# Kernel tuning notes

Measured on AMD Instinct MI355X. Metric: run time of the kernel, lower is better.

Reference implementation:

```python
import jax, jax.numpy as jnp
import numpy as np
from jax import lax

DN = ('NCHW', 'OIHW', 'NCHW')

def _dwsep(x, dw, pw_w, pw_b, stride):
    # depthwise: groups = in_channels, kernel (C,1,3,3)
    y = lax.conv_general_dilated(x, dw, (stride, stride), [(1, 1), (1, 1)],
                                 dimension_numbers=DN, feature_group_count=x.shape[1])
    # pointwise 1x1
    y = lax.conv_general_dilated(y, pw_w, (1, 1), 'VALID', dimension_numbers=DN)
    return y + pw_b[None, :, None, None]

def setup_inputs() -> dict:
    key = jax.random.key(0)
    ks = jax.random.split(key, 16)
    s = 0.1
    inp = {
        'flow_raw': jax.random.normal(ks[0], (32, 2, 480, 640), jnp.float32),
        'dw1': jax.random.normal(ks[1], (5, 1, 3, 3), jnp.float32) * s,
        'pw1_w': jax.random.normal(ks[2], (32, 5, 1, 1), jnp.float32) * s,
        'pw1_b': jnp.zeros((32,), jnp.float32),
        'dw2': jax.random.normal(ks[3], (32, 1, 3, 3), jnp.float32) * s,
        'pw2_w': jax.random.normal(ks[4], (64, 32, 1, 1), jnp.float32) * s,
        'pw2_b': jnp.zeros((64,), jnp.float32),
        'dw3': jax.random.normal(ks[5], (64, 1, 3, 3), jnp.float32) * s,
        'pw3_w': jax.random.normal(ks[6], (64, 64, 1, 1), jnp.float32) * s,
        'pw3_b': jnp.zeros((64,), jnp.float32),
        'attn_w': jax.random.normal(ks[7], (1, 64, 1, 1), jnp.float32) * s,
        'attn_b': jnp.zeros((1,), jnp.float32),
        'mlp1_w': jax.random.normal(ks[8], (32, 64), jnp.float32) * s,
        'mlp1_b': jnp.zeros((32,), jnp.float32),
        'mlp2_w': jax.random.normal(ks[9], (3, 32), jnp.float32) * s,
        'mlp2_b': jnp.zeros((3,), jnp.float32),
        'w_ih': jax.random.normal(ks[10], (96, 3), jnp.float32) * s,
        'w_hh': jax.random.normal(ks[11], (96, 32), jnp.float32) * s,
        'b_ih': jnp.zeros((96,), jnp.float32),
        'b_hh': jnp.zeros((96,), jnp.float32),
        'fc_w': jnp.zeros((3, 32), jnp.float32),  # gru_fc init to zero in torch code
        'fc_b': jnp.zeros((3,), jnp.float32),
    }
    return inp

def reference(flow_raw, dw1, pw1_w, pw1_b, dw2, pw2_w, pw2_b, dw3, pw3_w, pw3_b,
              attn_w, attn_b, mlp1_w, mlp1_b, mlp2_w, mlp2_b,
              w_ih, w_hh, b_ih, b_hh, fc_w, fc_b):
    B, _, H, W = flow_raw.shape
    # coordinate channels (x, y, r^2)
    y = jnp.linspace(-1.0, 1.0, H)
    x = jnp.linspace(-1.0, 1.0, W)
    yy, xx = jnp.meshgrid(y, x, indexing='ij')
    coords = jnp.stack([xx, yy, xx**2 + yy**2], axis=0)            # (3,H,W)
    coords_b = jnp.broadcast_to(coords[None], (B, 3, H, W))
    inp = jnp.concatenate([flow_raw, coords_b], axis=1)            # (B,5,H,W)

    f = jax.nn.elu(_dwsep(inp, dw1, pw1_w, pw1_b, 2))              # (B,32,H/2,W/2)
    f = jax.nn.elu(_dwsep(f, dw2, pw2_w, pw2_b, 2))                # (B,64,H/4,W/4)
    f = jax.nn.elu(_dwsep(f, dw3, pw3_w, pw3_b, 2))                # (B,64,H/8,W/8)

    # attention pooling
    logits = jnp.einsum('bchw,oc->bohw', f, attn_w[:, :, 0, 0]) + attn_b[None, :, None, None]
    Bs, _, Hs, Ws = logits.shape
    w = jax.nn.softmax(logits.reshape(Bs, Hs * Ws), axis=-1)       # (B, HW)
    pooled = jnp.einsum('bcn,bn->bc', f.reshape(Bs, 64, Hs * Ws), w)  # (B,64)

    # omega MLP
    h1 = jax.nn.elu(pooled @ mlp1_w.T + mlp1_b)
    omega_inst = h1 @ mlp2_w.T + mlp2_b                            # (B,3)

    # single-step GRU, h0 = 0 (PyTorch gate order: r, z, n)
    h0 = jnp.zeros((B, 32), flow_raw.dtype)
    gi = omega_inst @ w_ih.T + b_ih                                # (B,96)
    gh = h0 @ w_hh.T + b_hh
    i_r, i_z, i_n = jnp.split(gi, 3, axis=-1)
    h_r, h_z, h_n = jnp.split(gh, 3, axis=-1)
    r = jax.nn.sigmoid(i_r + h_r)
    z = jax.nn.sigmoid(i_z + h_z)
    n = jnp.tanh(i_n + r * h_n)
    h = (1.0 - z) * n + z * h0                                     # (B,32)

    delta_omega = h @ fc_w.T + fc_b
    return omega_inst + delta_omega
```

## Files before the change

kernel.cpp:

```cpp
#include <hip/hip_runtime.h>
#include <hip/hip_bf16.h>

#define H0 480
#define W0 640
#define H1 240
#define W1 320
#define H2 120
#define W2 160
#define H3 60
#define W3 80

#define W_PW1T  0
#define W_PW2T  160
#define W_PW3T  2208
#define WBUF_BYTES 65536

#define F2_PB (64 * H2 * W2)
#define F3_PB (64 * H3 * W3)

__global__ __launch_bounds__(256) void k_cvt(
    const float* __restrict__ pw1, const float* __restrict__ pw2,
    const float* __restrict__ pw3, float* __restrict__ wb)
{
    int t = threadIdx.x;
    for (int i = t; i < 160;  i += 256) { int o = i / 5,  c = i % 5;  wb[W_PW1T + c*32 + o] = pw1[i]; }
    for (int i = t; i < 2048; i += 256) { int o = i >> 5, c = i & 31; wb[W_PW2T + c*64 + o] = pw2[i]; }
    for (int i = t; i < 4096; i += 256) { int o = i >> 6, c = i & 63; wb[W_PW3T + c*64 + o] = pw3[i]; }
}

__global__ __launch_bounds__(256, 3) void k_fuse12(
    const float* __restrict__ flow, const float* __restrict__ dw1,
    const float* __restrict__ b1, const float* __restrict__ dw2,
    const float* __restrict__ b2, const float* __restrict__ wb,
    float* __restrict__ out)
{
    int idx = blockIdx.x * 256 + threadIdx.x;
    int ow = idx % W2; int tmp = idx / W2; int oh = tmp % H2; int b = tmp / H2;

    int fh0 = 2*oh - 1, fw0 = 2*ow - 1;
    const float sy = 2.f / (H0 - 1), sx = 2.f / (W0 - 1);

    float d[9][5];
    float vm[9];

    #pragma unroll
    for (int r = 0; r < 3; r++) {
        #pragma unroll
        for (int s = 0; s < 3; s++) {
            int p = r*3 + s;
            int fh = fh0 + r, fw = fw0 + s;
            vm[p] = (fh >= 0 && fw >= 0) ? 1.f : 0.f;
            int fhc = fh < 0 ? 0 : fh, fwc = fw < 0 ? 0 : fw;
            int ih0 = 2*fhc - 1, iw0 = 2*fwc - 1;
            float mh[3] = { ih0 >= 0 ? 1.f : 0.f, 1.f, 1.f };
            float mw[3] = { iw0 >= 0 ? 1.f : 0.f, 1.f, 1.f };
            int ihx[3] = { ih0 < 0 ? 0 : ih0, ih0 + 1, ih0 + 2 };
            int iwx[3] = { iw0 < 0 ? 0 : iw0, iw0 + 1, iw0 + 2 };

            #pragma unroll
            for (int c = 0; c < 2; c++) {
                const float* base = flow + ((size_t)(b*2 + c)) * (H0*W0);
                float a = 0.f;
                #pragma unroll
                for (int ky = 0; ky < 3; ky++) {
                    const float* rp = base + (size_t)ihx[ky] * W0;
                    #pragma unroll
                    for (int kx = 0; kx < 3; kx++)
                        a = fmaf(dw1[c*9 + ky*3 + kx], (mh[ky]*mw[kx]) * rp[iwx[kx]], a);
                }
                d[p][c] = a;
            }
            float ax = 0.f, ay = 0.f, ar = 0.f;
            #pragma unroll
            for (int ky = 0; ky < 3; ky++) {
                float yv = fmaf((float)(ih0 + ky), sy, -1.f);
                #pragma unroll
                for (int kx = 0; kx < 3; kx++) {
                    float xv = fmaf((float)(iw0 + kx), sx, -1.f);
                    float m = mh[ky] * mw[kx];
                    ax = fmaf(dw1[18 + ky*3 + kx], m * xv, ax);
                    ay = fmaf(dw1[27 + ky*3 + kx], m * yv, ay);
                    ar = fmaf(dw1[36 + ky*3 + kx], m * (xv*xv + yv*yv), ar);
                }
            }
            d[p][2] = ax; d[p][3] = ay; d[p][4] = ar;
        }
    }

    float acc[64];
    #pragma unroll
    for (int o = 0; o < 64; o++) acc[o] = b2[o];

    for (int c = 0; c < 32; c++) {
        const float* w1 = wb + W_PW1T + c;
        float w10 = w1[0], w11 = w1[32], w12 = w1[64], w13 = w1[96], w14 = w1[128];
        float bc = b1[c];
        const float* w9 = dw2 + c*9;
        float dv = 0.f;
        #pragma unroll
        for (int p = 0; p < 9; p++) {
            float v = bc;
            v = fmaf(w10, d[p][0], v);
            v = fmaf(w11, d[p][1], v);
            v = fmaf(w12, d[p][2], v);
            v = fmaf(w13, d[p][3], v);
            v = fmaf(w14, d[p][4], v);
            float f1v = v > 0.f ? v : (__expf(v) - 1.f);
            dv = fmaf(w9[p], f1v * vm[p], dv);
        }
        const float* wr = wb + W_PW2T + c*64;
        #pragma unroll
        for (int o = 0; o < 64; o++) acc[o] = fmaf(wr[o], dv, acc[o]);
    }

    size_t obase = ((size_t)b * 64) * (H2*W2) + (size_t)oh*W2 + ow;
    #pragma unroll
    for (int o = 0; o < 64; o++) {
        float v = acc[o];
        out[obase + (size_t)o*(H2*W2)] = v > 0.f ? v : (__expf(v) - 1.f);
    }
}

__global__ __launch_bounds__(256, 4) void k_stage3(
    const float* __restrict__ in, const float* __restrict__ dw3,
    const float* __restrict__ b3, const float* __restrict__ wb,
    float* __restrict__ out)
{
    int idx = blockIdx.x * 256 + threadIdx.x;
    int ow = idx % W3; int tmp = idx / W3; int oh = tmp % H3; int b = tmp / H3;
    int ih0 = 2*oh - 1, iw0 = 2*ow - 1;
    float mh[3] = { ih0 >= 0 ? 1.f : 0.f, 1.f, 1.f };
    float mw[3] = { iw0 >= 0 ? 1.f : 0.f, 1.f, 1.f };
    int ihx[3] = { ih0 < 0 ? 0 : ih0, ih0 + 1, ih0 + 2 };
    int iwx[3] = { iw0 < 0 ? 0 : iw0, iw0 + 1, iw0 + 2 };
    float m9[9];
    int off[9];
    #pragma unroll
    for (int ky = 0; ky < 3; ky++)
        #pragma unroll
        for (int kx = 0; kx < 3; kx++) {
            m9[ky*3 + kx] = mh[ky] * mw[kx];
            off[ky*3 + kx] = ihx[ky]*W2 + iwx[kx];
        }

    float acc[64];
    #pragma unroll
    for (int o = 0; o < 64; o++) acc[o] = b3[o];

    const float* inb = in + (size_t)b * F2_PB;
    for (int c = 0; c < 64; c++) {
        const float* g = inb + (size_t)c * (H2*W2);
        const float* w9 = dw3 + c*9;
        float dv = 0.f;
        #pragma unroll
        for (int p = 0; p < 9; p++)
            dv = fmaf(w9[p], m9[p] * g[off[p]], dv);
        const float* wr = wb + W_PW3T + c*64;
        #pragma unroll
        for (int o = 0; o < 64; o++) acc[o] = fmaf(wr[o], dv, acc[o]);
    }

    size_t obase = ((size_t)b * 64) * (H3*W3) + (size_t)oh*W3 + ow;
    #pragma unroll
    for (int o = 0; o < 64; o++) {
        float v = acc[o];
        out[obase + (size_t)o*(H3*W3)] = v > 0.f ? v : (__expf(v) - 1.f);
    }
}

__global__ __launch_bounds__(1024) void k_head(
    const float* __restrict__ f3,
    const float* __restrict__ attn_w, const float* __restrict__ attn_b,
    const float* __restrict__ mlp1_w, const float* __restrict__ mlp1_b,
    const float* __restrict__ mlp2_w, const float* __restrict__ mlp2_b,
    const float* __restrict__ w_ih, const float* __restrict__ b_ih,
    const float* __restrict__ b_hh,
    const float* __restrict__ fc_w, const float* __restrict__ fc_b,
    float* __restrict__ out)
{
    const int N  = H3 * W3;
    const int N4 = N / 4;
    __shared__ float s_w[H3 * W3];
    __shared__ float s_attn[64];
    __shared__ float s_redm[16];
    __shared__ float s_reds[16];
    __shared__ float s_inv[1];
    __shared__ float s_pooled[64];
    __shared__ float s_h1[32];
    __shared__ float s_om[3];
    __shared__ float s_h[32];

    int t = threadIdx.x, b = blockIdx.x;
    int lane = t & 63, wid = t >> 6;
    if (t < 64) s_attn[t] = attn_w[t];
    __syncthreads();

    const float4* fb4 = (const float4*)(f3 + (size_t)b * F3_PB);
    float ab = attn_b[0];

    float lmax = -1e30f;
    for (int n4 = t; n4 < N4; n4 += 1024) {
        float4 l = make_float4(ab, ab, ab, ab);
        #pragma unroll 8
        for (int c = 0; c < 64; c++) {
            float4 v = fb4[c * N4 + n4];
            float a = s_attn[c];
            l.x = fmaf(a, v.x, l.x); l.y = fmaf(a, v.y, l.y);
            l.z = fmaf(a, v.z, l.z); l.w = fmaf(a, v.w, l.w);
        }
        ((float4*)s_w)[n4] = l;
        lmax = fmaxf(lmax, fmaxf(fmaxf(l.x, l.y), fmaxf(l.z, l.w)));
    }
    #pragma unroll
    for (int off = 32; off; off >>= 1) lmax = fmaxf(lmax, __shfl_down(lmax, off, 64));
    if (lane == 0) s_redm[wid] = lmax;
    __syncthreads();
    {
        float m = s_redm[0];
        #pragma unroll
        for (int i = 1; i < 16; i++) m = fmaxf(m, s_redm[i]);
        lmax = m;
    }

    float lsum = 0.f;
    for (int n = t; n < N; n += 1024) { float e = __expf(s_w[n] - lmax); s_w[n] = e; lsum += e; }
    #pragma unroll
    for (int off = 32; off; off >>= 1) lsum += __shfl_down(lsum, off, 64);
    if (lane == 0) s_reds[wid] = lsum;
    __syncthreads();
    if (t == 0) {
        float s = 0.f;
        #pragma unroll
        for (int i = 0; i < 16; i++) s += s_reds[i];
        s_inv[0] = 1.f / s;
    }
    __syncthreads();
    float invS = s_inv[0];

    const float4* sw4 = (const float4*)s_w;
    for (int c = wid; c < 64; c += 16) {
        float s = 0.f;
        for (int i = lane; i < N4; i += 64) {
            float4 v = fb4[c * N4 + i];
            float4 w = sw4[i];
            s = fmaf(v.x, w.x, s); s = fmaf(v.y, w.y, s);
            s = fmaf(v.z, w.z, s); s = fmaf(v.w, w.w, s);
        }
        #pragma unroll
        for (int off = 32; off; off >>= 1) s += __shfl_down(s, off, 64);
        if (lane == 0) s_pooled[c] = s * invS;
    }
    __syncthreads();

    if (t < 32) {
        float a = mlp1_b[t];
        #pragma unroll 8
        for (int c = 0; c < 64; c++) a = fmaf(mlp1_w[t*64 + c], s_pooled[c], a);
        s_h1[t] = a > 0.f ? a : (__expf(a) - 1.f);
    }
    __syncthreads();
    if (t < 3) {
        float a = mlp2_b[t];
        for (int j = 0; j < 32; j++) a = fmaf(mlp2_w[t*32 + j], s_h1[j], a);
        s_om[t] = a;
    }
    __syncthreads();
    if (t < 32) {
        float gr = b_ih[t], gz = b_ih[32 + t], gn = b_ih[64 + t];
        #pragma unroll
        for (int k = 0; k < 3; k++) {
            float ok = s_om[k];
            gr = fmaf(w_ih[t*3 + k],        ok, gr);
            gz = fmaf(w_ih[(32 + t)*3 + k], ok, gz);
            gn = fmaf(w_ih[(64 + t)*3 + k], ok, gn);
        }
        float hr = b_hh[t], hz = b_hh[32 + t], hn = b_hh[64 + t];
        float r = 1.f / (1.f + __expf(-(gr + hr)));
        float z = 1.f / (1.f + __expf(-(gz + hz)));
        float nn = tanhf(gn + r * hn);
        s_h[t] = (1.f - z) * nn;
    }
    __syncthreads();
    if (t < 3) {
        float dl = fc_b[t];
        for (int j = 0; j < 32; j++) dl = fmaf(fc_w[t*32 + j], s_h[j], dl);
        out[b*3 + t] = s_om[t] + dl;
    }
}

extern "C" void kernel_launch(void* const* d_in, const int* in_sizes, int n_in,
                              void* d_out, int out_size, void* d_ws, size_t ws_size,
                              hipStream_t stream)
{
    const float* flow = (const float*)d_in[0];
    float* wb = (float*)d_ws;

    float* f2 = (float*)((char*)d_ws + WBUF_BYTES);
    float* f3 = f2 + (size_t)32 * F2_PB;

    k_cvt<<<1, 256, 0, stream>>>(
        (const float*)d_in[2], (const float*)d_in[5], (const float*)d_in[8], wb);

    k_fuse12<<<(32*H2*W2)/256, 256, 0, stream>>>(
        flow, (const float*)d_in[1], (const float*)d_in[3],
        (const float*)d_in[4], (const float*)d_in[6], wb, f2);

    k_stage3<<<(32*H3*W3)/256, 256, 0, stream>>>(
        f2, (const float*)d_in[7], (const float*)d_in[9], wb, f3);

    k_head<<<32, 1024, 0, stream>>>(f3,
        (const float*)d_in[10], (const float*)d_in[11],
        (const float*)d_in[12], (const float*)d_in[13],
        (const float*)d_in[14], (const float*)d_in[15],
        (const float*)d_in[16], (const float*)d_in[18],
        (const float*)d_in[19], (const float*)d_in[20],
        (const float*)d_in[21], (float*)d_out);
}
```

Measured before the change: 346.8 us.

## Split interior and border pixels; use packed FMA and factored coordinate convolution

Both conv kernels now remap thread indices so interior output pixels take a branch-free path without padding masks or clamped indices, and border pixels keep the original masked code. In stage 1 the interior path loads a shared 7x7 input window once per channel instead of re-gathering 9 overlapping 3x3 patches, and computes the x/y/r² coordinate-channel convolutions through separable row and column sums. The 64-wide pointwise accumulation uses 2-wide float vectors with elementwise FMA, intended to map to packed FP32 FMA. The cost is a larger code body and divergence inside warps that straddle the interior/border boundary.

Result: slower. 368.1 us (+6.1%).

```diff
diff --git a/kernel.cpp b/kernel.cpp
--- a/kernel.cpp
+++ b/kernel.cpp
@@ -17,6 +17,8 @@
 
 #define F2_PB (64 * H2 * W2)
 #define F3_PB (64 * H3 * W3)
+
+typedef float v2f __attribute__((ext_vector_type(2)));
 
 __global__ __launch_bounds__(256) void k_cvt(
     const float* __restrict__ pw1, const float* __restrict__ pw2,
@@ -35,89 +37,215 @@
     float* __restrict__ out)
 {
     int idx = blockIdx.x * 256 + threadIdx.x;
-    int ow = idx % W2; int tmp = idx / W2; int oh = tmp % H2; int b = tmp / H2;
-
-    int fh0 = 2*oh - 1, fw0 = 2*ow - 1;
+    int t = idx % (H2*W2); int b = idx / (H2*W2);
     const float sy = 2.f / (H0 - 1), sx = 2.f / (W0 - 1);
-
-    float d[9][5];
-    float vm[9];
-
-    #pragma unroll
-    for (int r = 0; r < 3; r++) {
-        #pragma unroll
-        for (int s = 0; s < 3; s++) {
-            int p = r*3 + s;
-            int fh = fh0 + r, fw = fw0 + s;
-            vm[p] = (fh >= 0 && fw >= 0) ? 1.f : 0.f;
-            int fhc = fh < 0 ? 0 : fh, fwc = fw < 0 ? 0 : fw;
-            int ih0 = 2*fhc - 1, iw0 = 2*fwc - 1;
-            float mh[3] = { ih0 >= 0 ? 1.f : 0.f, 1.f, 1.f };
-            float mw[3] = { iw0 >= 0 ? 1.f : 0.f, 1.f, 1.f };
-            int ihx[3] = { ih0 < 0 ? 0 : ih0, ih0 + 1, ih0 + 2 };
-            int iwx[3] = { iw0 < 0 ? 0 : iw0, iw0 + 1, iw0 + 2 };
-
+    const int NI = (H2-1) * (W2-1);
+
+    if (t < NI) {
+        int oh = 1 + t / (W2-1), ow = 1 + t % (W2-1);
+        float d[9][5];
+
+        {
+            const float* a0 = flow + ((size_t)(b*2)) * (H0*W0)
+                              + (size_t)(4*oh - 3) * W0 + (4*ow - 3);
             #pragma unroll
             for (int c = 0; c < 2; c++) {
-                const float* base = flow + ((size_t)(b*2 + c)) * (H0*W0);
-                float a = 0.f;
+                const float* ap = a0 + (size_t)c * (H0*W0);
+                float w[7][7];
+                #pragma unroll
+                for (int r7 = 0; r7 < 7; r7++)
+                    #pragma unroll
+                    for (int k = 0; k < 7; k++)
+                        w[r7][k] = ap[r7*W0 + k];
+                #pragma unroll
+                for (int r = 0; r < 3; r++)
+                    #pragma unroll
+                    for (int s = 0; s < 3; s++) {
+                        float a = 0.f;
+                        #pragma unroll
+                        for (int ky = 0; ky < 3; ky++)
+                            #pragma unroll
+                            for (int kx = 0; kx < 3; kx++)
+                                a = fmaf(dw1[c*9 + ky*3 + kx], w[2*r+ky][2*s+kx], a);
+                        d[r*3+s][c] = a;
+                    }
+            }
+        }
+
+        {
+            float cs2[3], rs3[3], cs4[3], rs4[3];
+            #pragma unroll
+            for (int k = 0; k < 3; k++) {
+                cs2[k] = dw1[18+k]   + dw1[21+k]   + dw1[24+k];
+                rs3[k] = dw1[27+3*k] + dw1[28+3*k] + dw1[29+3*k];
+                cs4[k] = dw1[36+k]   + dw1[39+k]   + dw1[42+k];
+                rs4[k] = dw1[36+3*k] + dw1[37+3*k] + dw1[38+3*k];
+            }
+            float u[7], vv7[7], u2[7], v2a[7];
+            float ub = fmaf((float)(4*ow - 3), sx, -1.f);
+            float vb = fmaf((float)(4*oh - 3), sy, -1.f);
+            #pragma unroll
+            for (int m = 0; m < 7; m++) {
+                u[m]   = fmaf((float)m, sx, ub);
+                vv7[m] = fmaf((float)m, sy, vb);
+                u2[m]  = u[m]*u[m];
+                v2a[m] = vv7[m]*vv7[m];
+            }
+            float axs[3], arx[3], ays[3], ary[3];
+            #pragma unroll
+            for (int s = 0; s < 3; s++) {
+                float ax = 0.f, gx = 0.f;
+                #pragma unroll
+                for (int kx = 0; kx < 3; kx++) {
+                    ax = fmaf(cs2[kx], u[2*s+kx],  ax);
+                    gx = fmaf(cs4[kx], u2[2*s+kx], gx);
+                }
+                axs[s] = ax; arx[s] = gx;
+            }
+            #pragma unroll
+            for (int r = 0; r < 3; r++) {
+                float ay = 0.f, gy = 0.f;
                 #pragma unroll
                 for (int ky = 0; ky < 3; ky++) {
-                    const float* rp = base + (size_t)ihx[ky] * W0;
+                    ay = fmaf(rs3[ky], vv7[2*r+ky], ay);
+                    gy = fmaf(rs4[ky], v2a[2*r+ky], gy);
+                }
+                ays[r] = ay; ary[r] = gy;
+            }
+            #pragma unroll
+            for (int r = 0; r < 3; r++)
+                #pragma unroll
+                for (int s = 0; s < 3; s++) {
+                    d[r*3+s][2] = axs[s];
+                    d[r*3+s][3] = ays[r];
+                    d[r*3+s][4] = arx[s] + ary[r];
+                }
+        }
+
+        v2f acc2[32];
+        #pragma unroll
+        for (int o = 0; o < 32; o++) acc2[o] = *(const v2f*)(b2 + 2*o);
+
+        for (int c = 0; c < 32; c++) {
+            const float* w1 = wb + W_PW1T + c;
+            float w10 = w1[0], w11 = w1[32], w12 = w1[64], w13 = w1[96], w14 = w1[128];
+            float bc = b1[c];
+            const float* w9 = dw2 + c*9;
+            float dv = 0.f;
+            #pragma unroll
+            for (int p = 0; p < 9; p++) {
+                float vv = bc;
+                vv = fmaf(w10, d[p][0], vv);
+                vv = fmaf(w11, d[p][1], vv);
+                vv = fmaf(w12, d[p][2], vv);
+                vv = fmaf(w13, d[p][3], vv);
+                vv = fmaf(w14, d[p][4], vv);
+                float f1v = vv > 0.f ? vv : (__expf(vv) - 1.f);
+                dv = fmaf(w9[p], f1v, dv);
+            }
+            const v2f* wr2 = (const v2f*)(wb + W_PW2T + c*64);
+            v2f dvv = { dv, dv };
+            #pragma unroll
+            for (int o = 0; o < 32; o++)
+                acc2[o] = __builtin_elementwise_fma(wr2[o], dvv, acc2[o]);
+        }
+
+        size_t obase = ((size_t)b * 64) * (H2*W2) + (size_t)oh*W2 + ow;
+        #pragma unroll
+        for (int o = 0; o < 32; o++) {
+            float va = acc2[o].x, vb2 = acc2[o].y;
+            out[obase + (size_t)(2*o)  *(H2*W2)] = va  > 0.f ? va  : (__expf(va)  - 1.f);
+            out[obase + (size_t)(2*o+1)*(H2*W2)] = vb2 > 0.f ? vb2 : (__expf(vb2) - 1.f);
+        }
+        return;
+    }
+
+    {
+        int s2 = t - NI;
+        int oh, ow;
+        if (s2 < W2) { oh = 0; ow = s2; } else { oh = s2 - (W2-1); ow = 0; }
+
+        int fh0 = 2*oh - 1, fw0 = 2*ow - 1;
+
+        float d[9][5];
+        float vm[9];
+
+        #pragma unroll
+        for (int r = 0; r < 3; r++) {
+            #pragma unroll
+            for (int s = 0; s < 3; s++) {
+                int p = r*3 + s;
+                int fh = fh0 + r, fw = fw0 + s;
+                vm[p] = (fh >= 0 && fw >= 0) ? 1.f : 0.f;
+                int fhc = fh < 0 ? 0 : fh, fwc = fw < 0 ? 0 : fw;
+                int ih0 = 2*fhc - 1, iw0 = 2*fwc - 1;
+                float mh[3] = { ih0 >= 0 ? 1.f : 0.f, 1.f, 1.f };
+                float mw[3] = { iw0 >= 0 ? 1.f : 0.f, 1.f, 1.f };
+                int ihx[3] = { ih0 < 0 ? 0 : ih0, ih0 + 1, ih0 + 2 };
+                int iwx[3] = { iw0 < 0 ? 0 : iw0, iw0 + 1, iw0 + 2 };
+
+                #pragma unroll
+                for (int c = 0; c < 2; c++) {
+                    const float* base = flow + ((size_t)(b*2 + c)) * (H0*W0);
+                    float a = 0.f;
                     #pragma unroll
-                    for (int kx = 0; kx < 3; kx++)
-                        a = fmaf(dw1[c*9 + ky*3 + kx], (mh[ky]*mw[kx]) * rp[iwx[kx]], a);
+                    for (int ky = 0; ky < 3; ky++) {
+                        const float* rp = base + (size_t)ihx[ky] * W0;
+                        #pragma unroll
+                        for (int kx = 0; kx < 3; kx++)
+                            a = fmaf(dw1[c*9 + ky*3 + kx], (mh[ky]*mw[kx]) * rp[iwx[kx]], a);
+                    }
+                    d[p][c] = a;
                 }
-                d[p][c] = a;
-            }
-            float ax = 0.f, ay = 0.f, ar = 0.f;
-            #pragma unroll
-            for (int ky = 0; ky < 3; ky++) {
-                float yv = fmaf((float)(ih0 + ky), sy, -1.f);
-                #pragma unroll
-                for (int kx = 0; kx < 3; kx++) {
-                    float xv = fmaf((float)(iw0 + kx), sx, -1.f);
-                    float m = mh[ky] * mw[kx];
-                    ax = fmaf(dw1[18 + ky*3 + kx], m * xv, ax);
-                    ay = fmaf(dw1[27 + ky*3 + kx], m * yv, ay);
-                    ar = fmaf(dw1[36 + ky*3 + kx], m * (xv*xv + yv*yv), ar);
+                float ax = 0.f, ay = 0.f, ar = 0.f;
+                #pragma unroll
+                for (int ky = 0; ky < 3; ky++) {
+                    float yv = fmaf((float)(ih0 + ky), sy, -1.f);
+                    #pragma unroll
+                    for (int kx = 0; kx < 3; kx++) {
+                        float xv = fmaf((float)(iw0 + kx), sx, -1.f);
+                        float m = mh[ky] * mw[kx];
+                        ax = fmaf(dw1[18 + ky*3 + kx], m * xv, ax);
+                        ay = fmaf(dw1[27 + ky*3 + kx], m * yv, ay);
+                        ar = fmaf(dw1[36 + ky*3 + kx], m * (xv*xv + yv*yv), ar);
+                    }
                 }
-            }
-            d[p][2] = ax; d[p][3] = ay; d[p][4] = ar;
-        }
-    }
-
-    float acc[64];
-    #pragma unroll
-    for (int o = 0; o < 64; o++) acc[o] = b2[o];
-
-    for (int c = 0; c < 32; c++) {
-        const float* w1 = wb + W_PW1T + c;
-        float w10 = w1[0], w11 = w1[32], w12 = w1[64], w13 = w1[96], w14 = w1[128];
-        float bc = b1[c];
-        const float* w9 = dw2 + c*9;
-        float dv = 0.f;
-        #pragma unroll
-        for (int p = 0; p < 9; p++) {
-            float v = bc;
-            v = fmaf(w10, d[p][0], v);
-            v = fmaf(w11, d[p][1], v);
-            v = fmaf(w12, d[p][2], v);
-            v = fmaf(w13, d[p][3], v);
-            v = fmaf(w14, d[p][4], v);
-            float f1v = v > 0.f ? v : (__expf(v) - 1.f);
-            dv = fmaf(w9[p], f1v * vm[p], dv);
-        }
-        const float* wr = wb + W_PW2T + c*64;
-        #pragma unroll
-        for (int o = 0; o < 64; o++) acc[o] = fmaf(wr[o], dv, acc[o]);
-    }
-
-    size_t obase = ((size_t)b * 64) * (H2*W2) + (size_t)oh*W2 + ow;
-    #pragma unroll
-    for (int o = 0; o < 64; o++) {
-        float v = acc[o];
-        out[obase + (size_t)o*(H2*W2)] = v > 0.f ? v : (__expf(v) - 1.f);
+                d[p][2] = ax; d[p][3] = ay; d[p][4] = ar;
+            }
+        }
+
+        float acc[64];
+        #pragma unroll
+        for (int o = 0; o < 64; o++) acc[o] = b2[o];
+
+        for (int c = 0; c < 32; c++) {
+            const float* w1 = wb + W_PW1T + c;
+            float w10 = w1[0], w11 = w1[32], w12 = w1[64], w13 = w1[96], w14 = w1[128];
+            float bc = b1[c];
+            const float* w9 = dw2 + c*9;
+            float dv = 0.f;
+            #pragma unroll
+            for (int p = 0; p < 9; p++) {
+                float v = bc;
+                v = fmaf(w10, d[p][0], v);
+                v = fmaf(w11, d[p][1], v);
+                v = fmaf(w12, d[p][2], v);
+                v = fmaf(w13, d[p][3], v);
+                v = fmaf(w14, d[p][4], v);
+                float f1v = v > 0.f ? v : (__expf(v) - 1.f);
+                dv = fmaf(w9[p], f1v * vm[p], dv);
+            }
+            const float* wr = wb + W_PW2T + c*64;
+            #pragma unroll
+            for (int o = 0; o < 64; o++) acc[o] = fmaf(wr[o], dv, acc[o]);
+        }
+
+        size_t obase = ((size_t)b * 64) * (H2*W2) + (size_t)oh*W2 + ow;
+        #pragma unroll
+        for (int o = 0; o < 64; o++) {
+            float v = acc[o];
+            out[obase + (size_t)o*(H2*W2)] = v > 0.f ? v : (__expf(v) - 1.f);
+        }
     }
 }
 
@@ -127,44 +255,86 @@
     float* __restrict__ out)
 {
     int idx = blockIdx.x * 256 + threadIdx.x;
-    int ow = idx % W3; int tmp = idx / W3; int oh = tmp % H3; int b = tmp / H3;
-    int ih0 = 2*oh - 1, iw0 = 2*ow - 1;
-    float mh[3] = { ih0 >= 0 ? 1.f : 0.f, 1.f, 1.f };
-    float mw[3] = { iw0 >= 0 ? 1.f : 0.f, 1.f, 1.f };
-    int ihx[3] = { ih0 < 0 ? 0 : ih0, ih0 + 1, ih0 + 2 };
-    int iwx[3] = { iw0 < 0 ? 0 : iw0, iw0 + 1, iw0 + 2 };
-    float m9[9];
-    int off[9];
-    #pragma unroll
-    for (int ky = 0; ky < 3; ky++)
-        #pragma unroll
-        for (int kx = 0; kx < 3; kx++) {
-            m9[ky*3 + kx] = mh[ky] * mw[kx];
-            off[ky*3 + kx] = ihx[ky]*W2 + iwx[kx];
-        }
-
-    float acc[64];
-    #pragma unroll
-    for (int o = 0; o < 64; o++) acc[o] = b3[o];
-
-    const float* inb = in + (size_t)b * F2_PB;
-    for (int c = 0; c < 64; c++) {
-        const float* g = inb + (size_t)c * (H2*W2);
-        const float* w9 = dw3 + c*9;
-        float dv = 0.f;
-        #pragma unroll
-        for (int p = 0; p < 9; p++)
-            dv = fmaf(w9[p], m9[p] * g[off[p]], dv);
-        const float* wr = wb + W_PW3T + c*64;
-        #pragma unroll
-        for (int o = 0; o < 64; o++) acc[o] = fmaf(wr[o], dv, acc[o]);
-    }
-
-    size_t obase = ((size_t)b * 64) * (H3*W3) + (size_t)oh*W3 + ow;
-    #pragma unroll
-    for (int o = 0; o < 64; o++) {
-        float v = acc[o];
-        out[obase + (size_t)o*(H3*W3)] = v > 0.f ? v : (__expf(v) - 1.f);
+    int t = idx % (H3*W3); int b = idx / (H3*W3);
+    const int NI = (H3-1) * (W3-1);
+
+    if (t < NI) {
+        int oh = 1 + t / (W3-1), ow = 1 + t % (W3-1);
+
+        v2f acc2[32];
+        #pragma unroll
+        for (int o = 0; o < 32; o++) acc2[o] = *(const v2f*)(b3 + 2*o);
+
+        const float* inb = in + (size_t)b * F2_PB + (size_t)(2*oh - 1)*W2 + (2*ow - 1);
+        for (int c = 0; c < 64; c++) {
+            const float* g = inb + (size_t)c * (H2*W2);
+            const float* w9 = dw3 + c*9;
+            float dv = 0.f;
+            #pragma unroll
+            for (int ky = 0; ky < 3; ky++)
+                #pragma unroll
+                for (int kx = 0; kx < 3; kx++)
+                    dv = fmaf(w9[ky*3 + kx], g[ky*W2 + kx], dv);
+            const v2f* wr2 = (const v2f*)(wb + W_PW3T + c*64);
+            v2f dvv = { dv, dv };
+            #pragma unroll
+            for (int o = 0; o < 32; o++)
+                acc2[o] = __builtin_elementwise_fma(wr2[o], dvv, acc2[o]);
+        }
+
+        size_t obase = ((size_t)b * 64) * (H3*W3) + (size_t)oh*W3 + ow;
+        #pragma unroll
+        for (int o = 0; o < 32; o++) {
+            float va = acc2[o].x, vb2 = acc2[o].y;
+            out[obase + (size_t)(2*o)  *(H3*W3)] = va  > 0.f ? va  : (__expf(va)  - 1.f);
+            out[obase + (size_t)(2*o+1)*(H3*W3)] = vb2 > 0.f ? vb2 : (__expf(vb2) - 1.f);
+        }
+        return;
+    }
+
+    {
+        int s2 = t - NI;
+        int oh, ow;
+        if (s2 < W3) { oh = 0; ow = s2; } else { oh = s2 - (W3-1); ow = 0; }
+
+        int ih0 = 2*oh - 1, iw0 = 2*ow - 1;
+        float mh[3] = { ih0 >= 0 ? 1.f : 0.f, 1.f, 1.f };
+        float mw[3] = { iw0 >= 0 ? 1.f : 0.f, 1.f, 1.f };
+        int ihx[3] = { ih0 < 0 ? 0 : ih0, ih0 + 1, ih0 + 2 };
+        int iwx[3] = { iw0 < 0 ? 0 : iw0, iw0 + 1, iw0 + 2 };
+        float m9[9];
+        int off[9];
+        #pragma unroll
+        for (int ky = 0; ky < 3; ky++)
+            #pragma unroll
+            for (int kx = 0; kx < 3; kx++) {
+                m9[ky*3 + kx] = mh[ky] * mw[kx];
+                off[ky*3 + kx] = ihx[ky]*W2 + iwx[kx];
+            }
+
+        float acc[64];
+        #pragma unroll
+        for (int o = 0; o < 64; o++) acc[o] = b3[o];
+
+        const float* inb = in + (size_t)b * F2_PB;
+        for (int c = 0; c < 64; c++) {
+            const float* g = inb + (size_t)c * (H2*W2);
+            const float* w9 = dw3 + c*9;
+            float dv = 0.f;
+            #pragma unroll
+            for (int p = 0; p < 9; p++)
+                dv = fmaf(w9[p], m9[p] * g[off[p]], dv);
+            const float* wr = wb + W_PW3T + c*64;
+            #pragma unroll
+            for (int o = 0; o < 64; o++) acc[o] = fmaf(wr[o], dv, acc[o]);
+        }
+
+        size_t obase = ((size_t)b * 64) * (H3*W3) + (size_t)oh*W3 + ow;
+        #pragma unroll
+        for (int o = 0; o < 64; o++) {
+            float v = acc[o];
+            out[obase + (size_t)o*(H3*W3)] = v > 0.f ? v : (__expf(v) - 1.f);
+        }
     }
 }
 
```

## Tile fused stage1-2 kernel with shared-memory f1 buffer to remove 9x recompute

Applied to the files above, without the earlier changes.

The fused depthwise/pointwise stage 1-2 kernel now processes 8x32 output tiles per block. It computes each stage-1 activation once into an LDS buffer laid out with even and odd columns split, instead of every thread recomputing nine neighbouring f1 values for all 32 channels. Coordinate-channel depthwise responses in the interior are folded into closed-form polynomials, and the 64-wide pointwise accumulate uses packed float2 FMAs. The cost is shared memory, barriers per 8-channel chunk, and extra boundary-handling code paths.

New measurement: 328.3 us. 5.3% less time.

```diff
diff --git a/kernel.cpp b/kernel.cpp
--- a/kernel.cpp
+++ b/kernel.cpp
@@ -17,6 +17,18 @@
 
 #define F2_PB (64 * H2 * W2)
 #define F3_PB (64 * H3 * W3)
+
+#define TH 8
+#define TW 32
+#define TILES_W 5
+#define TILES_H 15
+#define TILES_PB 75
+#define F1COLS 65
+#define NP 1105
+#define LROW 66
+#define LCH 1122
+
+typedef float v2f __attribute__((ext_vector_type(2)));
 
 __global__ __launch_bounds__(256) void k_cvt(
     const float* __restrict__ pw1, const float* __restrict__ pw2,
@@ -34,90 +46,169 @@
     const float* __restrict__ b2, const float* __restrict__ wb,
     float* __restrict__ out)
 {
-    int idx = blockIdx.x * 256 + threadIdx.x;
-    int ow = idx % W2; int tmp = idx / W2; int oh = tmp % H2; int b = tmp / H2;
-
-    int fh0 = 2*oh - 1, fw0 = 2*ow - 1;
-    const float sy = 2.f / (H0 - 1), sx = 2.f / (W0 - 1);
-
-    float d[9][5];
-    float vm[9];
-
-    #pragma unroll
-    for (int r = 0; r < 3; r++) {
-        #pragma unroll
-        for (int s = 0; s < 3; s++) {
-            int p = r*3 + s;
-            int fh = fh0 + r, fw = fw0 + s;
-            vm[p] = (fh >= 0 && fw >= 0) ? 1.f : 0.f;
-            int fhc = fh < 0 ? 0 : fh, fwc = fw < 0 ? 0 : fw;
-            int ih0 = 2*fhc - 1, iw0 = 2*fwc - 1;
+    __shared__ float f1buf[8 * LCH];
+
+    const int t = threadIdx.x;
+    const int bid = blockIdx.x;
+    const int b = bid / TILES_PB;
+    const int tile = bid - b * TILES_PB;
+    const int oh0 = (tile / TILES_W) * TH;
+    const int ow0 = (tile % TILES_W) * TW;
+
+    const float sx = 2.f / (W0 - 1), sy = 2.f / (H0 - 1);
+
+    float cs2[3], rs3[3], cs4[3], rs4[3];
+    #pragma unroll
+    for (int k = 0; k < 3; k++) {
+        cs2[k] = dw1[18+k]   + dw1[21+k]   + dw1[24+k];
+        rs3[k] = dw1[27+3*k] + dw1[28+3*k] + dw1[29+3*k];
+        cs4[k] = dw1[36+k]   + dw1[39+k]   + dw1[42+k];
+        rs4[k] = dw1[36+3*k] + dw1[37+3*k] + dw1[38+3*k];
+    }
+    const float ax2 = 2.f * sx, ay2 = 2.f * sy;
+    float ex[3], fyc[3];
+    #pragma unroll
+    for (int k = 0; k < 3; k++) { ex[k] = sx*(float)(k-1) - 1.f; fyc[k] = sy*(float)(k-1) - 1.f; }
+    const float AX1 = ax2*(cs2[0]+cs2[1]+cs2[2]);
+    const float AX0 = cs2[0]*ex[0]+cs2[1]*ex[1]+cs2[2]*ex[2];
+    const float AY1 = ay2*(rs3[0]+rs3[1]+rs3[2]);
+    const float AY0 = rs3[0]*fyc[0]+rs3[1]*fyc[1]+rs3[2]*fyc[2];
+    const float GX2 = ax2*ax2*(cs4[0]+cs4[1]+cs4[2]);
+    const float GX1 = 2.f*ax2*(cs4[0]*ex[0]+cs4[1]*ex[1]+cs4[2]*ex[2]);
+    const float GX0 = cs4[0]*ex[0]*ex[0]+cs4[1]*ex[1]*ex[1]+cs4[2]*ex[2]*ex[2];
+    const float GY2 = ay2*ay2*(rs4[0]+rs4[1]+rs4[2]);
+    const float GY1 = 2.f*ay2*(rs4[0]*fyc[0]+rs4[1]*fyc[1]+rs4[2]*fyc[2]);
+    const float GY0 = rs4[0]*fyc[0]*fyc[0]+rs4[1]*fyc[1]*fyc[1]+rs4[2]*fyc[2]*fyc[2];
+
+    float dd[5][5];
+    float vmf[5];
+    int   widx[5];
+    const float* fb0 = flow + (size_t)(b*2) * (H0*W0);
+    const float* fb1 = fb0 + (size_t)(H0*W0);
+
+    #pragma unroll
+    for (int i = 0; i < 5; i++) {
+        int p = t + i*256; if (p > NP-1) p = NP-1;
+        int tr = p / F1COLS;
+        int tc = p - tr * F1COLS;
+        widx[i] = tr*LROW + (tc & 1)*33 + (tc >> 1);
+        int fr = 2*oh0 - 1 + tr;
+        int fc = 2*ow0 - 1 + tc;
+        vmf[i] = (fr >= 0 && fc >= 0) ? 1.f : 0.f;
+        if (fr >= 1 && fc >= 1) {
+            const float* r0 = fb0 + (size_t)(2*fr - 1) * W0 + (2*fc - 1);
+            const float* r1 = fb1 + (size_t)(2*fr - 1) * W0 + (2*fc - 1);
+            float a0 = 0.f, a1 = 0.f;
+            #pragma unroll
+            for (int ky = 0; ky < 3; ky++)
+                #pragma unroll
+                for (int kx = 0; kx < 3; kx++) {
+                    a0 = fmaf(dw1[ky*3+kx],   r0[ky*W0+kx], a0);
+                    a1 = fmaf(dw1[9+ky*3+kx], r1[ky*W0+kx], a1);
+                }
+            dd[i][0] = a0; dd[i][1] = a1;
+            float fcf = (float)fc, frf = (float)fr;
+            dd[i][2] = fmaf(AX1, fcf, AX0);
+            dd[i][3] = fmaf(AY1, frf, AY0);
+            dd[i][4] = fmaf(fmaf(GX2, fcf, GX1), fcf, GX0)
+                     + fmaf(fmaf(GY2, frf, GY1), frf, GY0);
+        } else {
+            int frc = fr < 0 ? 0 : fr, fcc = fc < 0 ? 0 : fc;
+            int ih0 = 2*frc - 1, iw0 = 2*fcc - 1;
             float mh[3] = { ih0 >= 0 ? 1.f : 0.f, 1.f, 1.f };
             float mw[3] = { iw0 >= 0 ? 1.f : 0.f, 1.f, 1.f };
             int ihx[3] = { ih0 < 0 ? 0 : ih0, ih0 + 1, ih0 + 2 };
             int iwx[3] = { iw0 < 0 ? 0 : iw0, iw0 + 1, iw0 + 2 };
-
-            #pragma unroll
-            for (int c = 0; c < 2; c++) {
-                const float* base = flow + ((size_t)(b*2 + c)) * (H0*W0);
-                float a = 0.f;
+            float a0 = 0.f, a1 = 0.f;
+            #pragma unroll
+            for (int ky = 0; ky < 3; ky++) {
+                const float* rp0 = fb0 + (size_t)ihx[ky] * W0;
+                const float* rp1 = fb1 + (size_t)ihx[ky] * W0;
                 #pragma unroll
-                for (int ky = 0; ky < 3; ky++) {
-                    const float* rp = base + (size_t)ihx[ky] * W0;
-                    #pragma unroll
-                    for (int kx = 0; kx < 3; kx++)
-                        a = fmaf(dw1[c*9 + ky*3 + kx], (mh[ky]*mw[kx]) * rp[iwx[kx]], a);
+                for (int kx = 0; kx < 3; kx++) {
+                    float m = mh[ky]*mw[kx];
+                    a0 = fmaf(dw1[ky*3+kx],   m * rp0[iwx[kx]], a0);
+                    a1 = fmaf(dw1[9+ky*3+kx], m * rp1[iwx[kx]], a1);
                 }
-                d[p][c] = a;
             }
-            float ax = 0.f, ay = 0.f, ar = 0.f;
+            dd[i][0] = a0; dd[i][1] = a1;
+            float axv = 0.f, ayv = 0.f, arv = 0.f;
             #pragma unroll
             for (int ky = 0; ky < 3; ky++) {
                 float yv = fmaf((float)(ih0 + ky), sy, -1.f);
                 #pragma unroll
                 for (int kx = 0; kx < 3; kx++) {
                     float xv = fmaf((float)(iw0 + kx), sx, -1.f);
-                    float m = mh[ky] * mw[kx];
-                    ax = fmaf(dw1[18 + ky*3 + kx], m * xv, ax);
-                    ay = fmaf(dw1[27 + ky*3 + kx], m * yv, ay);
-                    ar = fmaf(dw1[36 + ky*3 + kx], m * (xv*xv + yv*yv), ar);
+                    float m = mh[ky]*mw[kx];
+                    axv = fmaf(dw1[18 + ky*3 + kx], m * xv, axv);
+                    ayv = fmaf(dw1[27 + ky*3 + kx], m * yv, ayv);
+                    arv = fmaf(dw1[36 + ky*3 + kx], m * (xv*xv + yv*yv), arv);
                 }
             }
-            d[p][2] = ax; d[p][3] = ay; d[p][4] = ar;
-        }
-    }
-
-    float acc[64];
-    #pragma unroll
-    for (int o = 0; o < 64; o++) acc[o] = b2[o];
-
-    for (int c = 0; c < 32; c++) {
-        const float* w1 = wb + W_PW1T + c;
-        float w10 = w1[0], w11 = w1[32], w12 = w1[64], w13 = w1[96], w14 = w1[128];
-        float bc = b1[c];
-        const float* w9 = dw2 + c*9;
-        float dv = 0.f;
-        #pragma unroll
-        for (int p = 0; p < 9; p++) {
-            float v = bc;
-            v = fmaf(w10, d[p][0], v);
-            v = fmaf(w11, d[p][1], v);
-            v = fmaf(w12, d[p][2], v);
-            v = fmaf(w13, d[p][3], v);
-            v = fmaf(w14, d[p][4], v);
-            float f1v = v > 0.f ? v : (__expf(v) - 1.f);
-            dv = fmaf(w9[p], f1v * vm[p], dv);
-        }
-        const float* wr = wb + W_PW2T + c*64;
-        #pragma unroll
-        for (int o = 0; o < 64; o++) acc[o] = fmaf(wr[o], dv, acc[o]);
-    }
-
-    size_t obase = ((size_t)b * 64) * (H2*W2) + (size_t)oh*W2 + ow;
-    #pragma unroll
-    for (int o = 0; o < 64; o++) {
-        float v = acc[o];
-        out[obase + (size_t)o*(H2*W2)] = v > 0.f ? v : (__expf(v) - 1.f);
+            dd[i][2] = axv; dd[i][3] = ayv; dd[i][4] = arv;
+        }
+    }
+
+    v2f acc2[32];
+    #pragma unroll
+    for (int o = 0; o < 32; o++) acc2[o] = *(const v2f*)(b2 + 2*o);
+
+    const int lr = t >> 5, lc = t & 31;
+    const int rbase = 2*lr*LROW + lc;
+
+    for (int cc = 0; cc < 4; cc++) {
+        #pragma unroll
+        for (int j = 0; j < 8; j++) {
+            int c = cc*8 + j;
+            float w10 = wb[W_PW1T + c];
+            float w11 = wb[W_PW1T + 32 + c];
+            float w12 = wb[W_PW1T + 64 + c];
+            float w13 = wb[W_PW1T + 96 + c];
+            float w14 = wb[W_PW1T + 128 + c];
+            float bc = b1[c];
+            #pragma unroll
+            for (int i = 0; i < 5; i++) {
+                float v = bc;
+                v = fmaf(w10, dd[i][0], v);
+                v = fmaf(w11, dd[i][1], v);
+                v = fmaf(w12, dd[i][2], v);
+                v = fmaf(w13, dd[i][3], v);
+                v = fmaf(w14, dd[i][4], v);
+                float f = v > 0.f ? v : (__expf(v) - 1.f);
+                f *= vmf[i];
+                if (i < 4)               f1buf[j*LCH + widx[i]] = f;
+                else if (t < NP - 1024)  f1buf[j*LCH + widx[4]] = f;
+            }
+        }
+        __syncthreads();
+        #pragma unroll
+        for (int j = 0; j < 8; j++) {
+            int c = cc*8 + j;
+            const float* w9 = dw2 + c*9;
+            const float* fp = f1buf + j*LCH + rbase;
+            float dv = 0.f;
+            #pragma unroll
+            for (int r = 0; r < 3; r++) {
+                dv = fmaf(w9[r*3+0], fp[r*LROW],      dv);
+                dv = fmaf(w9[r*3+1], fp[r*LROW + 33], dv);
+                dv = fmaf(w9[r*3+2], fp[r*LROW + 1],  dv);
+            }
+            const v2f* wr2 = (const v2f*)(wb + W_PW2T + c*64);
+            v2f dvv = { dv, dv };
+            #pragma unroll
+            for (int o = 0; o < 32; o++)
+                acc2[o] = __builtin_elementwise_fma(wr2[o], dvv, acc2[o]);
+        }
+        __syncthreads();
+    }
+
+    const int oh = oh0 + lr, ow = ow0 + lc;
+    size_t obase = ((size_t)b * 64) * (H2*W2) + (size_t)oh * W2 + ow;
+    #pragma unroll
+    for (int o = 0; o < 32; o++) {
+        float va = acc2[o].x, vb2 = acc2[o].y;
+        out[obase + (size_t)(2*o)   * (H2*W2)] = va  > 0.f ? va  : (__expf(va)  - 1.f);
+        out[obase + (size_t)(2*o+1) * (H2*W2)] = vb2 > 0.f ? vb2 : (__expf(vb2) - 1.f);
     }
 }
 
@@ -301,7 +392,7 @@
     k_cvt<<<1, 256, 0, stream>>>(
         (const float*)d_in[2], (const float*)d_in[5], (const float*)d_in[8], wb);
 
-    k_fuse12<<<(32*H2*W2)/256, 256, 0, stream>>>(
+    k_fuse12<<<32 * TILES_PB, 256, 0, stream>>>(
         flow, (const float*)d_in[1], (const float*)d_in[3],
         (const float*)d_in[4], (const float*)d_in[6], wb, f2);
 
```
